# Kernel optimization log

Measured on AMD Instinct MI355X. Metric: run time of the kernel, lower is better.

Reference implementation:

```python
import jax, jax.numpy as jnp
import numpy as np

D_IN, D_SC, DM, DS, NC, T, NS, MD = 1536, 234, 64, 8, 234, 12, 20, 8
B = 4096
LN_EPS = 1e-5


def setup_inputs() -> dict:
    key = jax.random.key(0)
    ks = jax.random.split(key, 16)
    r = lambda k, s: (jax.random.normal(k, s, jnp.float32) * 0.02)
    a_log = jnp.log(jnp.tile(jnp.arange(1, DS + 1, dtype=jnp.float32), (DM, 1)))  # (DM, DS)
    return {
        "emb": jax.random.normal(ks[0], (B, T, D_IN), jnp.float32),
        "scores": jax.random.uniform(ks[1], (B, T, D_SC), jnp.float32),
        "site_ids": jax.random.randint(ks[2], (B,), 0, NS),
        "hours": jax.random.randint(ks[3], (B,), 0, 24),
        "W_in": r(ks[4], (D_IN + D_SC, DM)), "b_in": jnp.zeros((DM,), jnp.float32),
        "ln_in_g": jnp.ones((DM,), jnp.float32), "ln_in_b": jnp.zeros((DM,), jnp.float32),
        "site_emb": r(ks[5], (NS, MD)), "hour_emb": r(ks[6], (24, MD)),
        "W_meta": r(ks[7], (2 * MD, DM)), "b_meta": jnp.zeros((DM,), jnp.float32),
        "pos_enc": r(ks[8], (1, T, DM)),
        "A_log_f": a_log, "Wp_f": r(ks[9], (DM, DM + 2 * DS)),
        "bp_f": jnp.zeros((DM + 2 * DS,), jnp.float32), "D_f": jnp.ones((DM,), jnp.float32),
        "A_log_b": a_log, "Wp_b": r(ks[10], (DM, DM + 2 * DS)),
        "bp_b": jnp.zeros((DM + 2 * DS,), jnp.float32), "D_b": jnp.ones((DM,), jnp.float32),
        "W_merge": r(ks[11], (2 * DM, DM)), "b_merge": jnp.zeros((DM,), jnp.float32),
        "ln_g": jnp.ones((DM,), jnp.float32), "ln_b": jnp.zeros((DM,), jnp.float32),
        "W_out": r(ks[12], (DM, NC)), "b_out": jnp.zeros((NC,), jnp.float32),
    }


def _ln(x, g, b):
    mu = x.mean(-1, keepdims=True)
    var = ((x - mu) ** 2).mean(-1, keepdims=True)
    return (x - mu) * jax.lax.rsqrt(var + LN_EPS) * g + b


def _selective_ssm(x, A_log, Wp, bp, D):
    # x: (B, T, DM); Mamba-style selective scan with ZOH discretization.
    proj = x @ Wp + bp                                # (B, T, DM+2*DS)
    delta = jax.nn.softplus(proj[..., :DM])           # (B, T, DM)
    Bc = proj[..., DM:DM + DS]                        # (B, T, DS)
    Cc = proj[..., DM + DS:]                          # (B, T, DS)
    A = -jnp.exp(A_log)                               # (DM, DS)
    dA = jnp.exp(delta[..., None] * A)                # (B, T, DM, DS)
    dBx = (delta * x)[..., None] * Bc[:, :, None, :]  # (B, T, DM, DS)

    def step(h, inp):
        dA_t, dBx_t, C_t = inp
        h = dA_t * h + dBx_t                          # (B, DM, DS)
        y = jnp.einsum('bdn,bn->bd', h, C_t)          # (B, DM)
        return h, y

    h0 = jnp.zeros((x.shape[0], DM, DS), x.dtype)
    _, ys = jax.lax.scan(step, h0, (dA.transpose(1, 0, 2, 3), dBx.transpose(1, 0, 2, 3), Cc.transpose(1, 0, 2)))
    return ys.transpose(1, 0, 2) + x * D              # (B, T, DM)


def reference(emb, scores, site_ids, hours, W_in, b_in, ln_in_g, ln_in_b, site_emb, hour_emb,
              W_meta, b_meta, pos_enc, A_log_f, Wp_f, bp_f, D_f, A_log_b, Wp_b, bp_b, D_b,
              W_merge, b_merge, ln_g, ln_b, W_out, b_out):
    x = jnp.concatenate([emb, scores], axis=-1)       # (B, T, D_IN+D_SC)
    h = jax.nn.gelu(_ln(x @ W_in + b_in, ln_in_g, ln_in_b), approximate=False)
    site_e = site_emb[jnp.clip(site_ids, 0, NS - 1)]  # (B, MD)
    hour_e = hour_emb[jnp.clip(hours, 0, 23)]         # (B, MD)
    meta = jnp.concatenate([site_e, hour_e], axis=-1) @ W_meta + b_meta
    h = h + meta[:, None, :] + pos_enc[:, :T, :]
    residual = h
    h_f = _selective_ssm(h, A_log_f, Wp_f, bp_f, D_f)
    h_b = _selective_ssm(h[:, ::-1, :], A_log_b, Wp_b, bp_b, D_b)[:, ::-1, :]
    h = jnp.concatenate([h_f, h_b], axis=-1) @ W_merge + b_merge
    h = _ln(h + residual, ln_g, ln_b)
    return h @ W_out + b_out                          # (B, T, NC)
```

## Files before the change

kernel.cpp:

```cpp
#include <hip/hip_runtime.h>
#include <hip/hip_bf16.h>

#define D_IN_ 1536
#define D_SC_ 234
#define DM_   64
#define NC_   234
#define T_    12
#define NS_   20
#define B_    4096
#define NROW_ (B_ * T_)
#define LN_EPS_ 1e-5f
#define PJS 164
#define RS_ 68

typedef __bf16 bf16x8 __attribute__((ext_vector_type(8)));
typedef float  f32x4  __attribute__((ext_vector_type(4)));

static __device__ __forceinline__ unsigned short f2bs(float f) {
    __hip_bfloat16 h = __float2bfloat16(f);
    return *reinterpret_cast<unsigned short*>(&h);
}
static __device__ __forceinline__ float bs2f(unsigned short u) {
    __hip_bfloat16 h = *reinterpret_cast<__hip_bfloat16*>(&u);
    return __bfloat162float(h);
}

__global__ void prep_w(const float* __restrict__ W_in, unsigned short* __restrict__ Wt) {
    int idx = blockIdx.x * 256 + threadIdx.x;
    if (idx >= 28 * 4096) return;
    int j = idx & 7, ln = (idx >> 3) & 63, nt = (idx >> 9) & 3, ks = (idx >> 11) & 1, kt = idx >> 12;
    int q = ln >> 4, mm = ln & 15;
    int n = nt * 16 + mm;
    int k = kt * 64 + ks * 32 + q * 8 + j;
    float v = (k < (D_IN_ + D_SC_)) ? W_in[k * 64 + n] : 0.0f;
    Wt[idx] = f2bs(v);
}

__global__ void prep_small(const float* __restrict__ Wp_f, const float* __restrict__ Wp_b,
                           const float* __restrict__ W_merge, const float* __restrict__ W_out,
                           unsigned short* __restrict__ Wpt, unsigned short* __restrict__ Wmt,
                           unsigned short* __restrict__ Wot) {
    int idx = blockIdx.x * 256 + threadIdx.x;
    if (idx >= 33792) return;
    int j = idx & 7, ln = (idx >> 3) & 63;
    int q = ln >> 4, mm = ln & 15;
    if (idx < 10240) {
        int tile = idx >> 9, nt = tile >> 1, ks = tile & 1;
        int n = nt * 16 + mm, k = ks * 32 + q * 8 + j;
        float v = (n >= 80) ? Wp_b[k * 80 + (n - 80)] : Wp_f[k * 80 + n];
        Wpt[idx] = f2bs(v);
    } else if (idx < 18432) {
        int i2 = idx - 10240;
        int tile = i2 >> 9, nt = tile >> 2, ks = tile & 3;
        int n = nt * 16 + mm, k = ks * 32 + q * 8 + j;
        Wmt[i2] = f2bs(W_merge[k * 64 + n]);
    } else {
        int i2 = idx - 18432;
        int tile = i2 >> 9, nt = tile >> 1, ks = tile & 1;
        int n = nt * 16 + mm, k = ks * 32 + q * 8 + j;
        Wot[i2] = f2bs((n < NC_) ? W_out[k * NC_ + n] : 0.0f);
    }
}

__global__ void prep_meta(const int* __restrict__ site_ids, const int* __restrict__ hours,
                          const float* __restrict__ site_emb, const float* __restrict__ hour_emb,
                          const float* __restrict__ W_meta, const float* __restrict__ b_meta,
                          unsigned short* __restrict__ meta_bf) {
    int idx = blockIdx.x * 256 + threadIdx.x;
    if (idx >= B_ * 64) return;
    int b = idx >> 6, n = idx & 63;
    int s = min(max(site_ids[b], 0), NS_ - 1);
    int h = min(max(hours[b], 0), 23);
    float acc = b_meta[n];
#pragma unroll
    for (int k = 0; k < 8; k++) acc += site_emb[s * 8 + k] * W_meta[k * 64 + n];
#pragma unroll
    for (int k = 0; k < 8; k++) acc += hour_emb[h * 8 + k] * W_meta[(8 + k) * 64 + n];
    meta_bf[idx] = f2bs(acc);
}

__launch_bounds__(256)
__global__ void k1_gemm(const float* __restrict__ emb, const float* __restrict__ scores,
                        const unsigned short* __restrict__ Wt,
                        const float* __restrict__ b_in, const float* __restrict__ ln_in_g,
                        const float* __restrict__ ln_in_b, const unsigned short* __restrict__ meta_bf,
                        const float* __restrict__ pos_enc, float* __restrict__ h_out) {
    const int tid  = threadIdx.x;
    const int lane = tid & 63;
    const int w    = tid >> 6;
    const int q    = lane >> 4;
    const int mm   = lane & 15;
    const int strip = blockIdx.x * 4 + w;
    const int row0  = strip * 16;

    const float* aptr = emb + (size_t)(row0 + mm) * D_IN_ + q * 8;
    const unsigned short* wptr = Wt + lane * 8;

    f32x4 acc[4];
#pragma unroll
    for (int nt = 0; nt < 4; nt++) acc[nt] = (f32x4){0.f, 0.f, 0.f, 0.f};

    float4 cur[4];
#pragma unroll
    for (int h = 0; h < 4; h++)
        cur[h] = *reinterpret_cast<const float4*>(aptr + (h >> 1) * 32 + (h & 1) * 4);

    __align__(16) unsigned short av[2][8];

    for (int kt = 0; kt < 23; kt++) {
        float4 nxt[4];
#pragma unroll
        for (int h = 0; h < 4; h++)
            nxt[h] = *reinterpret_cast<const float4*>(aptr + (kt + 1) * 64 + (h >> 1) * 32 + (h & 1) * 4);
        bf16x8 bfr[2][4];
#pragma unroll
        for (int ks = 0; ks < 2; ks++)
#pragma unroll
            for (int nt = 0; nt < 4; nt++)
                bfr[ks][nt] = *reinterpret_cast<const bf16x8*>(wptr + kt * 4096 + ks * 2048 + nt * 512);
#pragma unroll
        for (int ks = 0; ks < 2; ks++) {
            const float* cf = reinterpret_cast<const float*>(&cur[ks * 2]);
#pragma unroll
            for (int j = 0; j < 8; j++) av[ks][j] = f2bs(cf[j]);
        }
#pragma unroll
        for (int ks = 0; ks < 2; ks++) {
            bf16x8 af = *reinterpret_cast<const bf16x8*>(av[ks]);
#pragma unroll
            for (int nt = 0; nt < 4; nt++)
                acc[nt] = __builtin_amdgcn_mfma_f32_16x16x32_bf16(af, bfr[ks][nt], acc[nt], 0, 0, 0);
        }
#pragma unroll
        for (int h = 0; h < 4; h++) cur[h] = nxt[h];
    }
    {
        const int kt = 23;
        bf16x8 bfr[2][4];
#pragma unroll
        for (int ks = 0; ks < 2; ks++)
#pragma unroll
            for (int nt = 0; nt < 4; nt++)
                bfr[ks][nt] = *reinterpret_cast<const bf16x8*>(wptr + kt * 4096 + ks * 2048 + nt * 512);
#pragma unroll
        for (int ks = 0; ks < 2; ks++) {
            const float* cf = reinterpret_cast<const float*>(&cur[ks * 2]);
#pragma unroll
            for (int j = 0; j < 8; j++) av[ks][j] = f2bs(cf[j]);
        }
#pragma unroll
        for (int ks = 0; ks < 2; ks++) {
            bf16x8 af = *reinterpret_cast<const bf16x8*>(av[ks]);
#pragma unroll
            for (int nt = 0; nt < 4; nt++)
                acc[nt] = __builtin_amdgcn_mfma_f32_16x16x32_bf16(af, bfr[ks][nt], acc[nt], 0, 0, 0);
        }
    }
    {
        const float* sp = scores + (size_t)(row0 + mm) * D_SC_;
#pragma unroll
        for (int kt2 = 0; kt2 < 4; kt2++) {
#pragma unroll
            for (int ks = 0; ks < 2; ks++) {
                int c0 = kt2 * 64 + ks * 32 + q * 8;
                __align__(16) unsigned short avt[8];
#pragma unroll
                for (int p = 0; p < 4; p++) {
                    int c = c0 + 2 * p;
                    float2 v;
                    if (c + 1 < D_SC_) v = *reinterpret_cast<const float2*>(sp + c);
                    else { v.x = 0.0f; v.y = 0.0f; }
                    avt[2 * p]     = f2bs(v.x);
                    avt[2 * p + 1] = f2bs(v.y);
                }
                bf16x8 af = *reinterpret_cast<const bf16x8*>(avt);
#pragma unroll
                for (int nt = 0; nt < 4; nt++) {
                    bf16x8 bv = *reinterpret_cast<const bf16x8*>(wptr + (24 + kt2) * 4096 + ks * 2048 + nt * 512);
                    acc[nt] = __builtin_amdgcn_mfma_f32_16x16x32_bf16(af, bv, acc[nt], 0, 0, 0);
                }
            }
        }
    }

    float binv[4], gl[4], bl[4];
#pragma unroll
    for (int nt = 0; nt < 4; nt++) {
        binv[nt] = b_in[nt * 16 + mm];
        gl[nt]   = ln_in_g[nt * 16 + mm];
        bl[nt]   = ln_in_b[nt * 16 + mm];
    }
#pragma unroll
    for (int nt = 0; nt < 4; nt++)
#pragma unroll
        for (int reg = 0; reg < 4; reg++) acc[nt][reg] += binv[nt];

    float sum[4], sq[4];
#pragma unroll
    for (int reg = 0; reg < 4; reg++) {
        sum[reg] = acc[0][reg] + acc[1][reg] + acc[2][reg] + acc[3][reg];
        sq[reg]  = acc[0][reg]*acc[0][reg] + acc[1][reg]*acc[1][reg]
                 + acc[2][reg]*acc[2][reg] + acc[3][reg]*acc[3][reg];
    }
#pragma unroll
    for (int m2 = 1; m2 <= 8; m2 <<= 1) {
#pragma unroll
        for (int reg = 0; reg < 4; reg++) {
            sum[reg] += __shfl_xor(sum[reg], m2);
            sq[reg]  += __shfl_xor(sq[reg], m2);
        }
    }
#pragma unroll
    for (int reg = 0; reg < 4; reg++) {
        float mu   = sum[reg] * 0.015625f;
        float var  = sq[reg] * 0.015625f - mu * mu;
        float rstd = rsqrtf(var + LN_EPS_);
        int row  = row0 + q * 4 + reg;
        int bidx = row / 12;
        int t    = row - bidx * 12;
        const unsigned short* mrow = meta_bf + (size_t)bidx * 64;
        const float* prow = pos_enc + t * 64;
#pragma unroll
        for (int nt = 0; nt < 4; nt++) {
            int n = nt * 16 + mm;
            float x  = (acc[nt][reg] - mu) * rstd * gl[nt] + bl[nt];
            float ge = 0.5f * x * (1.0f + erff(x * 0.70710678118654752f));
            h_out[(size_t)row * 64 + n] = ge + bs2f(mrow[n]) + prow[n];
        }
    }
}

__launch_bounds__(256)
__global__ void k2_ssm(const float* __restrict__ h_in,
                       const float* __restrict__ A_log_f, const float* __restrict__ bp_f,
                       const float* __restrict__ D_f,
                       const float* __restrict__ A_log_b, const float* __restrict__ bp_b,
                       const float* __restrict__ D_b,
                       const unsigned short* __restrict__ Wpt, const unsigned short* __restrict__ Wmt,
                       const unsigned short* __restrict__ Wot,
                       const float* __restrict__ b_merge, const float* __restrict__ ln_g,
                       const float* __restrict__ ln_b, const float* __restrict__ b_out,
                       float* __restrict__ out) {
    __shared__ float h_s[T_ * 64];
    __shared__ __align__(16) unsigned short hb_s[1024];
    __shared__ float proj_s[T_ * PJS];
    __shared__ __align__(16) unsigned short yb_s[2048];
    __shared__ float r_s[T_ * RS_];
    __shared__ __align__(16) unsigned short gb_s[1024];

    const int tid  = threadIdx.x;
    const int lane = tid & 63;
    const int w    = tid >> 6;
    const int q    = lane >> 4;
    const int mm   = lane & 15;
    const int b    = blockIdx.x;

    if (tid < 192) {
        float4 hv = reinterpret_cast<const float4*>(h_in + (size_t)b * (T_ * 64))[tid];
        *reinterpret_cast<float4*>(&h_s[tid * 4]) = hv;
        int m = tid >> 4, c0 = (tid & 15) * 4;
        int base = (c0 >> 5) * 512 + (((c0 >> 3) & 3) * 16 + m) * 8 + (c0 & 7);
        hb_s[base + 0] = f2bs(hv.x);
        hb_s[base + 1] = f2bs(hv.y);
        hb_s[base + 2] = f2bs(hv.z);
        hb_s[base + 3] = f2bs(hv.w);
    }
    __syncthreads();

    {
        bf16x8 a0 = *reinterpret_cast<const bf16x8*>(&hb_s[lane * 8]);
        bf16x8 a1 = *reinterpret_cast<const bf16x8*>(&hb_s[512 + lane * 8]);
#pragma unroll
        for (int i = 0; i < 3; i++) {
            int nt = w + i * 4;
            if (nt < 10) {
                bf16x8 b0 = *reinterpret_cast<const bf16x8*>(Wpt + (nt * 2 + 0) * 512 + lane * 8);
                bf16x8 b1 = *reinterpret_cast<const bf16x8*>(Wpt + (nt * 2 + 1) * 512 + lane * 8);
                f32x4 c = (f32x4){0.f, 0.f, 0.f, 0.f};
                c = __builtin_amdgcn_mfma_f32_16x16x32_bf16(a0, b0, c, 0, 0, 0);
                c = __builtin_amdgcn_mfma_f32_16x16x32_bf16(a1, b1, c, 0, 0, 0);
                int n = nt * 16 + mm;
                float bpv = (n >= 80) ? bp_b[n - 80] : bp_f[n];
                if (q < 3) {
#pragma unroll
                    for (int reg = 0; reg < 4; reg++)
                        proj_s[(q * 4 + reg) * PJS + n] = c[reg] + bpv;
                }
            }
        }
    }
    __syncthreads();

    if (tid < 128) {
        int dir = tid >> 6, d = tid & 63;
        const float* Alog = dir ? A_log_b : A_log_f;
        const float* Dp   = dir ? D_b : D_f;
        float a[8];
#pragma unroll
        for (int n = 0; n < 8; n++) a[n] = -__expf(Alog[d * 8 + n]);
        float Dd = Dp[d];
        float st[8];
#pragma unroll
        for (int n = 0; n < 8; n++) st[n] = 0.0f;
        for (int t = 0; t < T_; t++) {
            int ts = dir ? (T_ - 1 - t) : t;
            float x    = h_s[ts * 64 + d];
            float draw = proj_s[ts * PJS + dir * 80 + d];
            float delta = (draw > 20.0f) ? draw : log1pf(__expf(draw));
            const float* pb = &proj_s[ts * PJS + dir * 80 + 64];
            float4 B0 = *reinterpret_cast<const float4*>(pb);
            float4 B1 = *reinterpret_cast<const float4*>(pb + 4);
            float4 C0 = *reinterpret_cast<const float4*>(pb + 8);
            float4 C1 = *reinterpret_cast<const float4*>(pb + 12);
            float Bv[8] = {B0.x, B0.y, B0.z, B0.w, B1.x, B1.y, B1.z, B1.w};
            float Cv[8] = {C0.x, C0.y, C0.z, C0.w, C1.x, C1.y, C1.z, C1.w};
            float dx = delta * x;
            float y = 0.0f;
#pragma unroll
            for (int n = 0; n < 8; n++) {
                st[n] = __expf(delta * a[n]) * st[n] + dx * Bv[n];
                y += st[n] * Cv[n];
            }
            float yv = y + x * Dd;
            int kk = dir * 64 + d;
            yb_s[(kk >> 5) * 512 + (((kk >> 3) & 3) * 16 + ts) * 8 + (kk & 7)] = f2bs(yv);
        }
    }
    __syncthreads();

    {
        int nt = w;
        f32x4 c = (f32x4){0.f, 0.f, 0.f, 0.f};
#pragma unroll
        for (int ks = 0; ks < 4; ks++) {
            bf16x8 A = *reinterpret_cast<const bf16x8*>(&yb_s[ks * 512 + lane * 8]);
            bf16x8 Bm = *reinterpret_cast<const bf16x8*>(Wmt + (nt * 4 + ks) * 512 + lane * 8);
            c = __builtin_amdgcn_mfma_f32_16x16x32_bf16(A, Bm, c, 0, 0, 0);
        }
        int n = nt * 16 + mm;
        float bm = b_merge[n];
        if (q < 3) {
#pragma unroll
            for (int reg = 0; reg < 4; reg++) {
                int t = q * 4 + reg;
                r_s[t * RS_ + n] = c[reg] + bm + h_s[t * 64 + n];
            }
        }
    }
    __syncthreads();

    {
        int j = lane;
#pragma unroll
        for (int i = 0; i < 3; i++) {
            int t = w + i * 4;
            float r  = r_s[t * RS_ + j];
            float s1 = r, s2 = r * r;
#pragma unroll
            for (int m2 = 1; m2 < 64; m2 <<= 1) { s1 += __shfl_xor(s1, m2); s2 += __shfl_xor(s2, m2); }
            float mu   = s1 * 0.015625f;
            float var  = s2 * 0.015625f - mu * mu;
            float rstd = rsqrtf(var + LN_EPS_);
            float g = (r - mu) * rstd * ln_g[j] + ln_b[j];
            gb_s[(j >> 5) * 512 + (((j >> 3) & 3) * 16 + t) * 8 + (j & 7)] = f2bs(g);
        }
    }
    __syncthreads();

    {
        bf16x8 a0 = *reinterpret_cast<const bf16x8*>(&gb_s[lane * 8]);
        bf16x8 a1 = *reinterpret_cast<const bf16x8*>(&gb_s[512 + lane * 8]);
#pragma unroll
        for (int i = 0; i < 4; i++) {
            int nt = w + i * 4;
            if (nt < 15) {
                bf16x8 b0 = *reinterpret_cast<const bf16x8*>(Wot + (nt * 2 + 0) * 512 + lane * 8);
                bf16x8 b1 = *reinterpret_cast<const bf16x8*>(Wot + (nt * 2 + 1) * 512 + lane * 8);
                f32x4 c = (f32x4){0.f, 0.f, 0.f, 0.f};
                c = __builtin_amdgcn_mfma_f32_16x16x32_bf16(a0, b0, c, 0, 0, 0);
                c = __builtin_amdgcn_mfma_f32_16x16x32_bf16(a1, b1, c, 0, 0, 0);
                int n = nt * 16 + mm;
                if (n < NC_) {
                    float bo = b_out[n];
                    if (q < 3) {
#pragma unroll
                        for (int reg = 0; reg < 4; reg++) {
                            int t = q * 4 + reg;
                            out[(size_t)b * (T_ * NC_) + t * NC_ + n] = c[reg] + bo;
                        }
                    }
                }
            }
        }
    }
}

extern "C" void kernel_launch(void* const* d_in, const int* in_sizes, int n_in,
                              void* d_out, int out_size, void* d_ws, size_t ws_size,
                              hipStream_t stream) {
    const float* emb      = (const float*)d_in[0];
    const float* scores   = (const float*)d_in[1];
    const int*   site_ids = (const int*)d_in[2];
    const int*   hours    = (const int*)d_in[3];
    const float* W_in     = (const float*)d_in[4];
    const float* b_in     = (const float*)d_in[5];
    const float* ln_in_g  = (const float*)d_in[6];
    const float* ln_in_b  = (const float*)d_in[7];
    const float* site_emb = (const float*)d_in[8];
    const float* hour_emb = (const float*)d_in[9];
    const float* W_meta   = (const float*)d_in[10];
    const float* b_meta   = (const float*)d_in[11];
    const float* pos_enc  = (const float*)d_in[12];
    const float* A_log_f  = (const float*)d_in[13];
    const float* Wp_f     = (const float*)d_in[14];
    const float* bp_f     = (const float*)d_in[15];
    const float* D_f      = (const float*)d_in[16];
    const float* A_log_b  = (const float*)d_in[17];
    const float* Wp_b     = (const float*)d_in[18];
    const float* bp_b     = (const float*)d_in[19];
    const float* D_b      = (const float*)d_in[20];
    const float* W_merge  = (const float*)d_in[21];
    const float* b_merge  = (const float*)d_in[22];
    const float* ln_g     = (const float*)d_in[23];
    const float* ln_b     = (const float*)d_in[24];
    const float* W_out    = (const float*)d_in[25];
    const float* b_out    = (const float*)d_in[26];

    char* ws = (char*)d_ws;
    unsigned short* Wt      = (unsigned short*)(ws + 0);
    unsigned short* meta_bf = (unsigned short*)(ws + 229376);
    unsigned short* Wpt     = (unsigned short*)(ws + 753664);
    unsigned short* Wmt     = (unsigned short*)(ws + 774144);
    unsigned short* Wot     = (unsigned short*)(ws + 790528);
    float*          h_ws    = (float*)(ws + 821248);

    prep_w      <<<448, 256, 0, stream>>>(W_in, Wt);
    prep_small  <<<132, 256, 0, stream>>>(Wp_f, Wp_b, W_merge, W_out, Wpt, Wmt, Wot);
    prep_meta   <<<1024, 256, 0, stream>>>(site_ids, hours, site_emb, hour_emb, W_meta, b_meta, meta_bf);
    k1_gemm     <<<768, 256, 0, stream>>>(emb, scores, Wt, b_in, ln_in_g, ln_in_b, meta_bf, pos_enc, h_ws);
    k2_ssm      <<<4096, 256, 0, stream>>>(h_ws, A_log_f, bp_f, D_f, A_log_b, bp_b, D_b,
                                           Wpt, Wmt, Wot, b_merge, ln_g, ln_b, b_out,
                                           (float*)d_out);
}
```

Measured before the change: 562.1 us.

## Process two batch items per SSM block and merge prep kernels into one

The three weight and metadata prep kernels become a single launch that dispatches on block index. The SSM kernel now handles two batch elements per 256-thread block, so all threads do useful scan work (previously only 128 of 256) and the MFMA tile loops are spread across more waves. It also reuses the bf16 input buffer for the LayerNorm output and drops the shared-memory row padding (PJS 164→160, RS 68→64). The costs are more shared memory per block, half as many blocks, and possible LDS bank conflicts now that the padding is gone.

```diff
diff --git a/kernel.cpp b/kernel.cpp
--- a/kernel.cpp
+++ b/kernel.cpp
@@ -10,8 +10,8 @@
 #define B_    4096
 #define NROW_ (B_ * T_)
 #define LN_EPS_ 1e-5f
-#define PJS 164
-#define RS_ 68
+#define PJS 160
+#define RS_ 64
 
 typedef __bf16 bf16x8 __attribute__((ext_vector_type(8)));
 typedef float  f32x4  __attribute__((ext_vector_type(4)));
@@ -25,58 +25,58 @@
     return __bfloat162float(h);
 }
 
-__global__ void prep_w(const float* __restrict__ W_in, unsigned short* __restrict__ Wt) {
-    int idx = blockIdx.x * 256 + threadIdx.x;
-    if (idx >= 28 * 4096) return;
-    int j = idx & 7, ln = (idx >> 3) & 63, nt = (idx >> 9) & 3, ks = (idx >> 11) & 1, kt = idx >> 12;
-    int q = ln >> 4, mm = ln & 15;
-    int n = nt * 16 + mm;
-    int k = kt * 64 + ks * 32 + q * 8 + j;
-    float v = (k < (D_IN_ + D_SC_)) ? W_in[k * 64 + n] : 0.0f;
-    Wt[idx] = f2bs(v);
-}
-
-__global__ void prep_small(const float* __restrict__ Wp_f, const float* __restrict__ Wp_b,
-                           const float* __restrict__ W_merge, const float* __restrict__ W_out,
-                           unsigned short* __restrict__ Wpt, unsigned short* __restrict__ Wmt,
-                           unsigned short* __restrict__ Wot) {
-    int idx = blockIdx.x * 256 + threadIdx.x;
-    if (idx >= 33792) return;
-    int j = idx & 7, ln = (idx >> 3) & 63;
-    int q = ln >> 4, mm = ln & 15;
-    if (idx < 10240) {
-        int tile = idx >> 9, nt = tile >> 1, ks = tile & 1;
-        int n = nt * 16 + mm, k = ks * 32 + q * 8 + j;
-        float v = (n >= 80) ? Wp_b[k * 80 + (n - 80)] : Wp_f[k * 80 + n];
-        Wpt[idx] = f2bs(v);
-    } else if (idx < 18432) {
-        int i2 = idx - 10240;
-        int tile = i2 >> 9, nt = tile >> 2, ks = tile & 3;
-        int n = nt * 16 + mm, k = ks * 32 + q * 8 + j;
-        Wmt[i2] = f2bs(W_merge[k * 64 + n]);
+__global__ void prep_all(const float* __restrict__ W_in,
+                         const float* __restrict__ Wp_f, const float* __restrict__ Wp_b,
+                         const float* __restrict__ W_merge, const float* __restrict__ W_out,
+                         const int* __restrict__ site_ids, const int* __restrict__ hours,
+                         const float* __restrict__ site_emb, const float* __restrict__ hour_emb,
+                         const float* __restrict__ W_meta, const float* __restrict__ b_meta,
+                         unsigned short* __restrict__ Wt, unsigned short* __restrict__ Wpt,
+                         unsigned short* __restrict__ Wmt, unsigned short* __restrict__ Wot,
+                         unsigned short* __restrict__ meta_bf) {
+    int blk = blockIdx.x, tid = threadIdx.x;
+    if (blk < 448) {
+        int idx = blk * 256 + tid;
+        int j = idx & 7, ln = (idx >> 3) & 63, nt = (idx >> 9) & 3, ks = (idx >> 11) & 1, kt = idx >> 12;
+        int q = ln >> 4, mm = ln & 15;
+        int n = nt * 16 + mm;
+        int k = kt * 64 + ks * 32 + q * 8 + j;
+        float v = (k < (D_IN_ + D_SC_)) ? W_in[k * 64 + n] : 0.0f;
+        Wt[idx] = f2bs(v);
+    } else if (blk < 580) {
+        int idx = (blk - 448) * 256 + tid;
+        if (idx >= 33792) return;
+        int j = idx & 7, ln = (idx >> 3) & 63;
+        int q = ln >> 4, mm = ln & 15;
+        if (idx < 10240) {
+            int tile = idx >> 9, nt = tile >> 1, ks = tile & 1;
+            int n = nt * 16 + mm, k = ks * 32 + q * 8 + j;
+            float v = (n >= 80) ? Wp_b[k * 80 + (n - 80)] : Wp_f[k * 80 + n];
+            Wpt[idx] = f2bs(v);
+        } else if (idx < 18432) {
+            int i2 = idx - 10240;
+            int tile = i2 >> 9, nt = tile >> 2, ks = tile & 3;
+            int n = nt * 16 + mm, k = ks * 32 + q * 8 + j;
+            Wmt[i2] = f2bs(W_merge[k * 64 + n]);
+        } else {
+            int i2 = idx - 18432;
+            int tile = i2 >> 9, nt = tile >> 1, ks = tile & 1;
+            int n = nt * 16 + mm, k = ks * 32 + q * 8 + j;
+            Wot[i2] = f2bs((n < NC_) ? W_out[k * NC_ + n] : 0.0f);
+        }
     } else {
-        int i2 = idx - 18432;
-        int tile = i2 >> 9, nt = tile >> 1, ks = tile & 1;
-        int n = nt * 16 + mm, k = ks * 32 + q * 8 + j;
-        Wot[i2] = f2bs((n < NC_) ? W_out[k * NC_ + n] : 0.0f);
-    }
-}
-
-__global__ void prep_meta(const int* __restrict__ site_ids, const int* __restrict__ hours,
-                          const float* __restrict__ site_emb, const float* __restrict__ hour_emb,
-                          const float* __restrict__ W_meta, const float* __restrict__ b_meta,
-                          unsigned short* __restrict__ meta_bf) {
-    int idx = blockIdx.x * 256 + threadIdx.x;
-    if (idx >= B_ * 64) return;
-    int b = idx >> 6, n = idx & 63;
-    int s = min(max(site_ids[b], 0), NS_ - 1);
-    int h = min(max(hours[b], 0), 23);
-    float acc = b_meta[n];
-#pragma unroll
-    for (int k = 0; k < 8; k++) acc += site_emb[s * 8 + k] * W_meta[k * 64 + n];
-#pragma unroll
-    for (int k = 0; k < 8; k++) acc += hour_emb[h * 8 + k] * W_meta[(8 + k) * 64 + n];
-    meta_bf[idx] = f2bs(acc);
+        int idx = (blk - 580) * 256 + tid;
+        if (idx >= B_ * 64) return;
+        int b = idx >> 6, n = idx & 63;
+        int s = min(max(site_ids[b], 0), NS_ - 1);
+        int h = min(max(hours[b], 0), 23);
+        float acc = b_meta[n];
+#pragma unroll
+        for (int k = 0; k < 8; k++) acc += site_emb[s * 8 + k] * W_meta[k * 64 + n];
+#pragma unroll
+        for (int k = 0; k < 8; k++) acc += hour_emb[h * 8 + k] * W_meta[(8 + k) * 64 + n];
+        meta_bf[idx] = f2bs(acc);
+    }
 }
 
 __launch_bounds__(256)
@@ -241,58 +241,66 @@
                        const float* __restrict__ b_merge, const float* __restrict__ ln_g,
                        const float* __restrict__ ln_b, const float* __restrict__ b_out,
                        float* __restrict__ out) {
-    __shared__ float h_s[T_ * 64];
-    __shared__ __align__(16) unsigned short hb_s[1024];
-    __shared__ float proj_s[T_ * PJS];
-    __shared__ __align__(16) unsigned short yb_s[2048];
-    __shared__ float r_s[T_ * RS_];
-    __shared__ __align__(16) unsigned short gb_s[1024];
+    __shared__ float h_s[2 * T_ * 64];
+    __shared__ __align__(16) unsigned short fb_s[2][1024];
+    __shared__ float proj_s[2][T_ * PJS];
+    __shared__ __align__(16) unsigned short yb_s[2][2048];
+    __shared__ float r_s[2][T_ * RS_];
 
     const int tid  = threadIdx.x;
     const int lane = tid & 63;
     const int w    = tid >> 6;
     const int q    = lane >> 4;
     const int mm   = lane & 15;
-    const int b    = blockIdx.x;
-
-    if (tid < 192) {
-        float4 hv = reinterpret_cast<const float4*>(h_in + (size_t)b * (T_ * 64))[tid];
-        *reinterpret_cast<float4*>(&h_s[tid * 4]) = hv;
-        int m = tid >> 4, c0 = (tid & 15) * 4;
-        int base = (c0 >> 5) * 512 + (((c0 >> 3) & 3) * 16 + m) * 8 + (c0 & 7);
-        hb_s[base + 0] = f2bs(hv.x);
-        hb_s[base + 1] = f2bs(hv.y);
-        hb_s[base + 2] = f2bs(hv.z);
-        hb_s[base + 3] = f2bs(hv.w);
+    const int b0   = blockIdx.x * 2;
+
+    const float4* hsrc = reinterpret_cast<const float4*>(h_in + (size_t)b0 * (T_ * 64));
+#pragma unroll
+    for (int it = 0; it < 2; it++) {
+        int i4 = tid + it * 256;
+        if (i4 < 384) {
+            float4 hv = hsrc[i4];
+            *reinterpret_cast<float4*>(&h_s[i4 * 4]) = hv;
+            int bb = i4 / 192, f4 = i4 - bb * 192;
+            int m = f4 >> 4, c0 = (f4 & 15) * 4;
+            int base = (c0 >> 5) * 512 + (((c0 >> 3) & 3) * 16 + m) * 8 + (c0 & 7);
+            fb_s[bb][base + 0] = f2bs(hv.x);
+            fb_s[bb][base + 1] = f2bs(hv.y);
+            fb_s[bb][base + 2] = f2bs(hv.z);
+            fb_s[bb][base + 3] = f2bs(hv.w);
+        }
     }
     __syncthreads();
 
     {
-        bf16x8 a0 = *reinterpret_cast<const bf16x8*>(&hb_s[lane * 8]);
-        bf16x8 a1 = *reinterpret_cast<const bf16x8*>(&hb_s[512 + lane * 8]);
-#pragma unroll
-        for (int i = 0; i < 3; i++) {
-            int nt = w + i * 4;
-            if (nt < 10) {
-                bf16x8 b0 = *reinterpret_cast<const bf16x8*>(Wpt + (nt * 2 + 0) * 512 + lane * 8);
-                bf16x8 b1 = *reinterpret_cast<const bf16x8*>(Wpt + (nt * 2 + 1) * 512 + lane * 8);
-                f32x4 c = (f32x4){0.f, 0.f, 0.f, 0.f};
-                c = __builtin_amdgcn_mfma_f32_16x16x32_bf16(a0, b0, c, 0, 0, 0);
-                c = __builtin_amdgcn_mfma_f32_16x16x32_bf16(a1, b1, c, 0, 0, 0);
-                int n = nt * 16 + mm;
-                float bpv = (n >= 80) ? bp_b[n - 80] : bp_f[n];
-                if (q < 3) {
-#pragma unroll
-                    for (int reg = 0; reg < 4; reg++)
-                        proj_s[(q * 4 + reg) * PJS + n] = c[reg] + bpv;
-                }
+        bf16x8 a[2][2];
+#pragma unroll
+        for (int bb = 0; bb < 2; bb++)
+#pragma unroll
+            for (int ks = 0; ks < 2; ks++)
+                a[bb][ks] = *reinterpret_cast<const bf16x8*>(&fb_s[bb][ks * 512 + lane * 8]);
+#pragma unroll
+        for (int i = 0; i < 5; i++) {
+            int cmb = w + i * 4;
+            int bb = cmb / 10, nt = cmb - bb * 10;
+            bf16x8 b0v = *reinterpret_cast<const bf16x8*>(Wpt + (nt * 2 + 0) * 512 + lane * 8);
+            bf16x8 b1v = *reinterpret_cast<const bf16x8*>(Wpt + (nt * 2 + 1) * 512 + lane * 8);
+            f32x4 c = (f32x4){0.f, 0.f, 0.f, 0.f};
+            c = __builtin_amdgcn_mfma_f32_16x16x32_bf16(a[bb][0], b0v, c, 0, 0, 0);
+            c = __builtin_amdgcn_mfma_f32_16x16x32_bf16(a[bb][1], b1v, c, 0, 0, 0);
+            int n = nt * 16 + mm;
+            float bpv = (n >= 80) ? bp_b[n - 80] : bp_f[n];
+            if (q < 3) {
+#pragma unroll
+                for (int reg = 0; reg < 4; reg++)
+                    proj_s[bb][(q * 4 + reg) * PJS + n] = c[reg] + bpv;
             }
         }
     }
     __syncthreads();
 
-    if (tid < 128) {
-        int dir = tid >> 6, d = tid & 63;
+    {
+        int bb = tid >> 7, dir = (tid >> 6) & 1, d = tid & 63;
         const float* Alog = dir ? A_log_b : A_log_f;
         const float* Dp   = dir ? D_b : D_f;
         float a[8];
@@ -302,12 +310,14 @@
         float st[8];
 #pragma unroll
         for (int n = 0; n < 8; n++) st[n] = 0.0f;
+        const float* hsb = h_s + bb * (T_ * 64);
+        const float* psb = proj_s[bb];
         for (int t = 0; t < T_; t++) {
             int ts = dir ? (T_ - 1 - t) : t;
-            float x    = h_s[ts * 64 + d];
-            float draw = proj_s[ts * PJS + dir * 80 + d];
+            float x    = hsb[ts * 64 + d];
+            float draw = psb[ts * PJS + dir * 80 + d];
             float delta = (draw > 20.0f) ? draw : log1pf(__expf(draw));
-            const float* pb = &proj_s[ts * PJS + dir * 80 + 64];
+            const float* pb = &psb[ts * PJS + dir * 80 + 64];
             float4 B0 = *reinterpret_cast<const float4*>(pb);
             float4 B1 = *reinterpret_cast<const float4*>(pb + 4);
             float4 C0 = *reinterpret_cast<const float4*>(pb + 8);
@@ -323,27 +333,31 @@
             }
             float yv = y + x * Dd;
             int kk = dir * 64 + d;
-            yb_s[(kk >> 5) * 512 + (((kk >> 3) & 3) * 16 + ts) * 8 + (kk & 7)] = f2bs(yv);
+            yb_s[bb][(kk >> 5) * 512 + (((kk >> 3) & 3) * 16 + ts) * 8 + (kk & 7)] = f2bs(yv);
         }
     }
     __syncthreads();
 
     {
-        int nt = w;
-        f32x4 c = (f32x4){0.f, 0.f, 0.f, 0.f};
-#pragma unroll
-        for (int ks = 0; ks < 4; ks++) {
-            bf16x8 A = *reinterpret_cast<const bf16x8*>(&yb_s[ks * 512 + lane * 8]);
-            bf16x8 Bm = *reinterpret_cast<const bf16x8*>(Wmt + (nt * 4 + ks) * 512 + lane * 8);
-            c = __builtin_amdgcn_mfma_f32_16x16x32_bf16(A, Bm, c, 0, 0, 0);
-        }
-        int n = nt * 16 + mm;
-        float bm = b_merge[n];
-        if (q < 3) {
-#pragma unroll
-            for (int reg = 0; reg < 4; reg++) {
-                int t = q * 4 + reg;
-                r_s[t * RS_ + n] = c[reg] + bm + h_s[t * 64 + n];
+#pragma unroll
+        for (int i = 0; i < 2; i++) {
+            int cmb = w + i * 4;
+            int bb = cmb >> 2, nt = cmb & 3;
+            f32x4 c = (f32x4){0.f, 0.f, 0.f, 0.f};
+#pragma unroll
+            for (int ks = 0; ks < 4; ks++) {
+                bf16x8 A  = *reinterpret_cast<const bf16x8*>(&yb_s[bb][ks * 512 + lane * 8]);
+                bf16x8 Bm = *reinterpret_cast<const bf16x8*>(Wmt + (nt * 4 + ks) * 512 + lane * 8);
+                c = __builtin_amdgcn_mfma_f32_16x16x32_bf16(A, Bm, c, 0, 0, 0);
+            }
+            int n = nt * 16 + mm;
+            float bm = b_merge[n];
+            if (q < 3) {
+#pragma unroll
+                for (int reg = 0; reg < 4; reg++) {
+                    int t = q * 4 + reg;
+                    r_s[bb][t * RS_ + n] = c[reg] + bm + h_s[bb * (T_ * 64) + t * 64 + n];
+                }
             }
         }
     }
@@ -352,9 +366,10 @@
     {
         int j = lane;
 #pragma unroll
-        for (int i = 0; i < 3; i++) {
-            int t = w + i * 4;
-            float r  = r_s[t * RS_ + j];
+        for (int i = 0; i < 6; i++) {
+            int rr = w + i * 4;
+            int bb = rr / 12, t = rr - bb * 12;
+            float r  = r_s[bb][t * RS_ + j];
             float s1 = r, s2 = r * r;
 #pragma unroll
             for (int m2 = 1; m2 < 64; m2 <<= 1) { s1 += __shfl_xor(s1, m2); s2 += __shfl_xor(s2, m2); }
@@ -362,23 +377,24 @@
             float var  = s2 * 0.015625f - mu * mu;
             float rstd = rsqrtf(var + LN_EPS_);
             float g = (r - mu) * rstd * ln_g[j] + ln_b[j];
-            gb_s[(j >> 5) * 512 + (((j >> 3) & 3) * 16 + t) * 8 + (j & 7)] = f2bs(g);
+            fb_s[bb][(j >> 5) * 512 + (((j >> 3) & 3) * 16 + t) * 8 + (j & 7)] = f2bs(g);
         }
     }
     __syncthreads();
 
     {
-        bf16x8 a0 = *reinterpret_cast<const bf16x8*>(&gb_s[lane * 8]);
-        bf16x8 a1 = *reinterpret_cast<const bf16x8*>(&gb_s[512 + lane * 8]);
-#pragma unroll
-        for (int i = 0; i < 4; i++) {
-            int nt = w + i * 4;
-            if (nt < 15) {
-                bf16x8 b0 = *reinterpret_cast<const bf16x8*>(Wot + (nt * 2 + 0) * 512 + lane * 8);
-                bf16x8 b1 = *reinterpret_cast<const bf16x8*>(Wot + (nt * 2 + 1) * 512 + lane * 8);
+#pragma unroll
+        for (int i = 0; i < 8; i++) {
+            int cmb = w + i * 4;
+            if (cmb < 30) {
+                int bb = cmb / 15, nt = cmb - bb * 15;
+                bf16x8 a0 = *reinterpret_cast<const bf16x8*>(&fb_s[bb][lane * 8]);
+                bf16x8 a1 = *reinterpret_cast<const bf16x8*>(&fb_s[bb][512 + lane * 8]);
+                bf16x8 b0v = *reinterpret_cast<const bf16x8*>(Wot + (nt * 2 + 0) * 512 + lane * 8);
+                bf16x8 b1v = *reinterpret_cast<const bf16x8*>(Wot + (nt * 2 + 1) * 512 + lane * 8);
                 f32x4 c = (f32x4){0.f, 0.f, 0.f, 0.f};
-                c = __builtin_amdgcn_mfma_f32_16x16x32_bf16(a0, b0, c, 0, 0, 0);
-                c = __builtin_amdgcn_mfma_f32_16x16x32_bf16(a1, b1, c, 0, 0, 0);
+                c = __builtin_amdgcn_mfma_f32_16x16x32_bf16(a0, b0v, c, 0, 0, 0);
+                c = __builtin_amdgcn_mfma_f32_16x16x32_bf16(a1, b1v, c, 0, 0, 0);
                 int n = nt * 16 + mm;
                 if (n < NC_) {
                     float bo = b_out[n];
@@ -386,7 +402,7 @@
 #pragma unroll
                         for (int reg = 0; reg < 4; reg++) {
                             int t = q * 4 + reg;
-                            out[(size_t)b * (T_ * NC_) + t * NC_ + n] = c[reg] + bo;
+                            out[(size_t)(b0 + bb) * (T_ * NC_) + t * NC_ + n] = c[reg] + bo;
                         }
                     }
                 }
@@ -434,11 +450,11 @@
     unsigned short* Wot     = (unsigned short*)(ws + 790528);
     float*          h_ws    = (float*)(ws + 821248);
 
-    prep_w      <<<448, 256, 0, stream>>>(W_in, Wt);
-    prep_small  <<<132, 256, 0, stream>>>(Wp_f, Wp_b, W_merge, W_out, Wpt, Wmt, Wot);
-    prep_meta   <<<1024, 256, 0, stream>>>(site_ids, hours, site_emb, hour_emb, W_meta, b_meta, meta_bf);
-    k1_gemm     <<<768, 256, 0, stream>>>(emb, scores, Wt, b_in, ln_in_g, ln_in_b, meta_bf, pos_enc, h_ws);
-    k2_ssm      <<<4096, 256, 0, stream>>>(h_ws, A_log_f, bp_f, D_f, A_log_b, bp_b, D_b,
-                                           Wpt, Wmt, Wot, b_merge, ln_g, ln_b, b_out,
-                                           (float*)d_out);
-}
+    prep_all <<<1604, 256, 0, stream>>>(W_in, Wp_f, Wp_b, W_merge, W_out,
+                                        site_ids, hours, site_emb, hour_emb, W_meta, b_meta,
+                                        Wt, Wpt, Wmt, Wot, meta_bf);
+    k1_gemm  <<<768, 256, 0, stream>>>(emb, scores, Wt, b_in, ln_in_g, ln_in_b, meta_bf, pos_enc, h_ws);
+    k2_ssm   <<<2048, 256, 0, stream>>>(h_ws, A_log_f, bp_f, D_f, A_log_b, bp_b, D_b,
+                                        Wpt, Wmt, Wot, b_merge, ln_g, ln_b, b_out,
+                                        (float*)d_out);
+}
```

Result: no change. 566.6 us (+0.8%).
